# Optimization experiments

Measured on AMD Instinct MI355X. Metric: run time of the kernel, lower is better.

Reference implementation:

```python
import jax, jax.numpy as jnp
import numpy as np

B, S, D_IN, HID, H, OUT = 4, 2048, 1024, 1024, 16, 128
DH = HID // H
SCALE = float(np.sqrt(DH))
ELEV, FLOOR2 = 4, 32


def setup_inputs() -> dict:
    key = jax.random.key(0)
    ks = jax.random.split(key, 12)
    w = lambda k, o, i: jax.random.normal(k, (o, i), dtype=jnp.float32) * 0.02
    b = lambda k, o: jax.random.normal(k, (o,), dtype=jnp.float32) * 0.02
    return {
        "query": jax.random.normal(ks[0], (B, S, D_IN), dtype=jnp.float32),
        "key": jax.random.normal(ks[1], (B, S, D_IN), dtype=jnp.float32),
        "value": jax.random.normal(ks[2], (B, S, D_IN), dtype=jnp.float32),
        "mask": jax.random.randint(ks[3], (B, 1, 1, S), 0, 2, dtype=jnp.int32),
        "wq_w": w(ks[4], HID, D_IN), "wq_b": b(ks[5], HID),
        "wk_w": w(ks[6], HID, D_IN), "wk_b": b(ks[7], HID),
        "wv_w": w(ks[8], HID, D_IN), "wv_b": b(ks[9], HID),
        "fc_w": w(ks[10], OUT, HID), "fc_b": b(ks[11], OUT),
    }


def reference(query, key, value, mask, wq_w, wq_b, wk_w, wk_b, wv_w, wv_b, fc_w, fc_b):
    bsz, seq = query.shape[0], query.shape[1]
    # torch Linear: x @ W.T + b
    split = lambda x: x.reshape(bsz, seq, H, DH).transpose(0, 2, 1, 3)  # (b,h,s,dh)
    Q = split(query @ wq_w.T + wq_b)
    K = split(key @ wk_w.T + wk_b)
    V = split(value @ wv_w.T + wv_b)
    energy = jnp.einsum('bhqd,bhkd->bhqk', Q, K) / SCALE
    energy = jnp.where(mask == 0, jnp.float32(-1e10), energy)
    attn = jax.nn.softmax(energy, axis=-1)  # dropout is identity in eval mode
    x = jnp.einsum('bhqk,bhkd->bhqd', attn, V)
    x = x.transpose(0, 2, 1, 3).reshape(bsz, seq, HID)
    x = x @ fc_w.T + fc_b
    x = x.reshape(-1, ELEV, FLOOR2)  # (b*s, elevator_num, floor_num*2)
    return jax.nn.softmax(x, axis=1)  # nn.Softmax(dim=1)
```

## Files before the change

kernel.cpp:

```cpp
#include <hip/hip_runtime.h>
#include <stdint.h>

#define S_LEN 2048
#define DK 1024
#define NH 16
#define DH 64
#define LOG2E 1.4426950408889634f
#define M_FIX 10.0f

typedef __attribute__((ext_vector_type(8))) short bf16x8;
typedef __attribute__((ext_vector_type(4))) float f32x4;

__device__ __forceinline__ unsigned short f2bf(float f) {
    union { float f; uint32_t u; } v; v.f = f;
    return (unsigned short)((v.u + 0x7fffu + ((v.u >> 16) & 1u)) >> 16);
}

__device__ __forceinline__ float fast_exp2(float x) {
#if __has_builtin(__builtin_amdgcn_exp2f)
    return __builtin_amdgcn_exp2f(x);
#else
    return exp2f(x);
#endif
}

__device__ __forceinline__ uint32_t cvt_pk_bf16(float a, float b) {
    uint32_t r;
    asm("v_cvt_pk_bf16_f32 %0, %1, %2" : "=v"(r) : "v"(a), "v"(b));
    return r;
}

__device__ __forceinline__ void gload_lds16(const void* g, void* l) {
    __builtin_amdgcn_global_load_lds((const __attribute__((address_space(1))) void*)g,
                                     (__attribute__((address_space(3))) void*)l, 16, 0, 0);
}

__global__ __launch_bounds__(256) void cvt7_kernel(
    const float* __restrict__ a0, const float* __restrict__ a1, const float* __restrict__ a2,
    const float* __restrict__ a3, const float* __restrict__ a4, const float* __restrict__ a5,
    const float* __restrict__ a6,
    unsigned short* __restrict__ o0, unsigned short* __restrict__ o1, unsigned short* __restrict__ o2,
    unsigned short* __restrict__ o3, unsigned short* __restrict__ o4, unsigned short* __restrict__ o5,
    unsigned short* __restrict__ o6,
    int n4_big, int n4_w, int n4_f)
{
    const int y = blockIdx.y;
    const float* in = (y == 0) ? a0 : (y == 1) ? a1 : (y == 2) ? a2 :
                      (y == 3) ? a3 : (y == 4) ? a4 : (y == 5) ? a5 : a6;
    unsigned short* out = (y == 0) ? o0 : (y == 1) ? o1 : (y == 2) ? o2 :
                          (y == 3) ? o3 : (y == 4) ? o4 : (y == 5) ? o5 : o6;
    const int n4 = (y < 3) ? n4_big : ((y < 6) ? n4_w : n4_f);
    const float4* pin = (const float4*)in;
    ushort4* pout = (ushort4*)out;
    int i = blockIdx.x * blockDim.x + threadIdx.x;
    int stride = gridDim.x * blockDim.x;
    for (; i < n4; i += stride) {
        float4 v = pin[i];
        ushort4 o;
        o.x = f2bf(v.x); o.y = f2bf(v.y); o.z = f2bf(v.z); o.w = f2bf(v.w);
        pout[i] = o;
    }
}

__global__ __launch_bounds__(512) void proj_gemm(
    const unsigned short* __restrict__ Xq, const unsigned short* __restrict__ Xk, const unsigned short* __restrict__ Xv,
    const unsigned short* __restrict__ Wq, const unsigned short* __restrict__ Wk, const unsigned short* __restrict__ Wv,
    const float* __restrict__ bq, const float* __restrict__ bk, const float* __restrict__ bv,
    unsigned short* __restrict__ Qh, unsigned short* __restrict__ Kh, unsigned short* __restrict__ Vt)
{
    const int d = blockIdx.x + (blockIdx.y << 3) + (blockIdx.z << 9);
    const int k = d & 7, s = d >> 3;
    const int nn = s & 7;
    const int mz = ((s >> 3) << 3) + k;
    const int m0 = (mz & 63) * 128;
    const int z = mz >> 6;

    const unsigned short* X = (z == 0) ? Xq : ((z == 1) ? Xk : Xv);
    const unsigned short* W = (z == 0) ? Wq : ((z == 1) ? Wk : Wv);
    const float* bias = (z == 0) ? bq : ((z == 1) ? bk : bv);

    const int n0 = nn * 128;
    const int tid = threadIdx.x;
    const int w = tid >> 6;
    const int l = tid & 63;
    const int wm = w >> 2, wn = w & 3;
    const int g = l >> 4, c = l & 15;

    __shared__ __align__(16) unsigned short As[2][2 * 128 * 32];
    __shared__ __align__(16) unsigned short Bs[2][2 * 128 * 32];

    f32x4 acc[4][2] = {};

    const int srow = l >> 2;
    const int schunk = (((l & 3) - (l >> 3)) & 3) * 8;

    const int sub = w >> 2;
    const int rb = 32 * (w & 3);

    auto stage = [&](int kk, int buf) {
#pragma unroll
        for (int i = 0; i < 2; ++i) {
            int r0 = rb + 16 * i;
            gload_lds16(X + (size_t)(m0 + r0 + srow) * DK + kk + 32 * sub + schunk,
                        &As[buf][sub * 4096 + r0 * 32]);
            gload_lds16(W + (size_t)(n0 + r0 + srow) * DK + kk + 32 * sub + schunk,
                        &Bs[buf][sub * 4096 + r0 * 32]);
        }
    };

    stage(0, 0);

    for (int t = 0; t < 16; ++t) {
        const int buf = t & 1;
        __syncthreads();

        if (t < 15) stage((t + 1) << 6, buf ^ 1);

        const int rchunk = 8 * ((g + (c >> 1)) & 3);
        __builtin_amdgcn_s_setprio(1);
#pragma unroll
        for (int k32 = 0; k32 < 2; ++k32) {
            bf16x8 a[4], bb[2];
#pragma unroll
            for (int mi = 0; mi < 4; ++mi)
                a[mi] = *(const bf16x8*)&As[buf][k32 * 4096 + (64 * wm + 16 * mi + c) * 32 + rchunk];
#pragma unroll
            for (int nj = 0; nj < 2; ++nj)
                bb[nj] = *(const bf16x8*)&Bs[buf][k32 * 4096 + (32 * wn + 16 * nj + c) * 32 + rchunk];
#pragma unroll
            for (int mi = 0; mi < 4; ++mi)
#pragma unroll
                for (int nj = 0; nj < 2; ++nj)
                    acc[mi][nj] = __builtin_amdgcn_mfma_f32_16x16x32_bf16(a[mi], bb[nj], acc[mi][nj], 0, 0, 0);
        }
        __builtin_amdgcn_s_setprio(0);
    }

    const float scale = (z == 0) ? (0.125f * LOG2E) : 1.0f;
#pragma unroll
    for (int mi = 0; mi < 4; ++mi) {
#pragma unroll
        for (int nj = 0; nj < 2; ++nj) {
            int col = n0 + 32 * wn + 16 * nj + c;
            float bval = bias[col];
            int h = col >> 6, dh = col & 63;
            int row0 = m0 + 64 * wm + 16 * mi + 4 * g;
            int b = row0 >> 11, ss = row0 & 2047;
            if (z != 2) {
                unsigned short* Out = (z == 0) ? Qh : Kh;
#pragma unroll
                for (int r = 0; r < 4; ++r) {
                    float v = (acc[mi][nj][r] + bval) * scale;
                    Out[((size_t)(b * NH + h) * S_LEN + (ss + r)) * DH + dh] = f2bf(v);
                }
            } else {
                ushort4 o;
                o.x = f2bf(acc[mi][nj][0] + bval);
                o.y = f2bf(acc[mi][nj][1] + bval);
                o.z = f2bf(acc[mi][nj][2] + bval);
                o.w = f2bf(acc[mi][nj][3] + bval);
                int q = (ss >> 2) & 7;
                int newpos = (ss & ~31) + 8 * (q & 3) + 4 * (q >> 2);
                *(ushort4*)&Vt[((size_t)(b * NH + h) * DH + dh) * S_LEN + newpos] = o;
            }
        }
    }
}

__global__ __launch_bounds__(256, 4) void attn_kernel(
    const unsigned short* __restrict__ Qh, const unsigned short* __restrict__ Kh,
    const unsigned short* __restrict__ Vt, const int* __restrict__ maskI,
    unsigned short* __restrict__ O)
{
    const int id = blockIdx.x + (blockIdx.y << 4);
    const int swzid = (id & 7) * 128 + (id >> 3);
    const int q0 = (swzid & 15) * 128;
    const int bh = swzid >> 4;
    const int b = bh >> 4, h = bh & 15;
    const int tid = threadIdx.x, w = tid >> 6, l = tid & 63;
    const int g = l >> 4, c = l & 15;

    __shared__ __align__(16) unsigned short Ks[2][4096];
    __shared__ __align__(16) unsigned short Vs[2][4096];
    __shared__ __align__(16) float mskA[S_LEN];

    bf16x8 qf[2][2];
    const size_t qbase = (size_t)bh * S_LEN + q0 + 32 * w;
#pragma unroll
    for (int mi = 0; mi < 2; ++mi)
#pragma unroll
        for (int k32 = 0; k32 < 2; ++k32)
            qf[mi][k32] = *(const bf16x8*)&Qh[(qbase + 16 * mi + c) * DH + k32 * 32 + 8 * g];

    f32x4 ao[2][4] = {};
    f32x4 ls[2] = {};
    bf16x8 ones;
#pragma unroll
    for (int j = 0; j < 8; ++j) ones[j] = (short)0x3F80;

    const int kswz = ((l & 7) ^ (l >> 3)) * 8;
    const int vrow = l >> 2;
    const int vsrc = (((l & 3) - (l >> 3)) & 3) * 8;

    auto stageKV = [&](int kv, int buf) {
#pragma unroll
        for (int u = 0; u < 2; ++u) {
            int kvs = kv + 32 * u;
            gload_lds16(Kh + ((size_t)bh * S_LEN + kvs + 8 * w + (l >> 3)) * DH + kswz,
                        &Ks[buf][u * 2048 + w * 512]);
            gload_lds16(Vt + ((size_t)bh * DH + 16 * w + vrow) * S_LEN + kvs + vsrc,
                        &Vs[buf][u * 2048 + w * 512]);
        }
    };

    stageKV(0, 0);
    {
        const int4* mp = (const int4*)(maskI + b * S_LEN);
#pragma unroll
        for (int i = 0; i < 2; ++i) {
            int idx = tid + 256 * i;
            int4 m = mp[idx];
            float4 f;
            f.x = m.x ? (-M_FIX * LOG2E) : -3e38f;
            f.y = m.y ? (-M_FIX * LOG2E) : -3e38f;
            f.z = m.z ? (-M_FIX * LOG2E) : -3e38f;
            f.w = m.w ? (-M_FIX * LOG2E) : -3e38f;
            *(float4*)&mskA[idx * 4] = f;
        }
    }

    for (int t = 0; t < 32; ++t) {
        const int cur = t & 1;
        const int kv0 = t << 6;
        __syncthreads();

        if (t < 31) stageKV(kv0 + 64, cur ^ 1);

#pragma unroll
        for (int u = 0; u < 2; ++u) {
            const int base = u * 2048;
            const int kv0s = kv0 + 32 * u;

            float4 mk0 = *(const float4*)&mskA[kv0s + 4 * g];
            float4 mk1 = *(const float4*)&mskA[kv0s + 16 + 4 * g];
            f32x4 sf[2][2];
            sf[0][0] = f32x4{mk0.x, mk0.y, mk0.z, mk0.w};
            sf[1][0] = sf[0][0];
            sf[0][1] = f32x4{mk1.x, mk1.y, mk1.z, mk1.w};
            sf[1][1] = sf[0][1];

            __builtin_amdgcn_s_setprio(1);
#pragma unroll
            for (int nj = 0; nj < 2; ++nj) {
                int krow = 16 * nj + c;
#pragma unroll
                for (int k32 = 0; k32 < 2; ++k32) {
                    int chunk = (k32 * 4 + g) ^ (krow & 7);
                    bf16x8 kf = *(const bf16x8*)&Ks[cur][base + krow * 64 + chunk * 8];
#pragma unroll
                    for (int mi = 0; mi < 2; ++mi)
                        sf[mi][nj] = __builtin_amdgcn_mfma_f32_16x16x32_bf16(kf, qf[mi][k32], sf[mi][nj], 0, 0, 0);
                }
            }
            __builtin_amdgcn_s_setprio(0);

            bf16x8 pf[2];
#pragma unroll
            for (int mi = 0; mi < 2; ++mi) {
                float e00 = fast_exp2(sf[mi][0][0]);
                float e01 = fast_exp2(sf[mi][0][1]);
                float e02 = fast_exp2(sf[mi][0][2]);
                float e03 = fast_exp2(sf[mi][0][3]);
                float e10 = fast_exp2(sf[mi][1][0]);
                float e11 = fast_exp2(sf[mi][1][1]);
                float e12 = fast_exp2(sf[mi][1][2]);
                float e13 = fast_exp2(sf[mi][1][3]);
                union { uint32_t u2[4]; bf16x8 v; } pu;
                pu.u2[0] = cvt_pk_bf16(e00, e01);
                pu.u2[1] = cvt_pk_bf16(e02, e03);
                pu.u2[2] = cvt_pk_bf16(e10, e11);
                pu.u2[3] = cvt_pk_bf16(e12, e13);
                pf[mi] = pu.v;
            }

            __builtin_amdgcn_s_setprio(1);
#pragma unroll
            for (int nc = 0; nc < 4; ++nc) {
                int row = 16 * nc + c;
                int s16 = (g + (c >> 1)) & 3;
                bf16x8 vf = *(const bf16x8*)&Vs[cur][base + row * 32 + 8 * s16];
#pragma unroll
                for (int mi = 0; mi < 2; ++mi)
                    ao[mi][nc] = __builtin_amdgcn_mfma_f32_16x16x32_bf16(pf[mi], vf, ao[mi][nc], 0, 0, 0);
            }
#pragma unroll
            for (int mi = 0; mi < 2; ++mi)
                ls[mi] = __builtin_amdgcn_mfma_f32_16x16x32_bf16(pf[mi], ones, ls[mi], 0, 0, 0);
            __builtin_amdgcn_s_setprio(0);
        }
    }

#pragma unroll
    for (int mi = 0; mi < 2; ++mi)
#pragma unroll
        for (int r = 0; r < 4; ++r) {
            int s = q0 + 32 * w + 16 * mi + 4 * g + r;
            float inv = 1.0f / ls[mi][r];
#pragma unroll
            for (int nc = 0; nc < 4; ++nc) {
                int dh = 16 * nc + c;
                O[(size_t)(b * S_LEN + s) * 1024 + h * DH + dh] = f2bf(ao[mi][nc][r] * inv);
            }
        }
}

__global__ __launch_bounds__(256) void fc_kernel(
    const unsigned short* __restrict__ O, const unsigned short* __restrict__ Wf,
    const float* __restrict__ bfc, float* __restrict__ out)
{
    const int m0 = blockIdx.x * 64;
    const int tid = threadIdx.x, w = tid >> 6, l = tid & 63;
    const int g = l >> 4, c = l & 15;

    __shared__ __align__(16) unsigned short As[3][64 * 32];
    __shared__ __align__(16) unsigned short Bs[3][128 * 32];

    f32x4 acc[8] = {};

    const int srow = l >> 2;
    const int schunk = (((l & 3) - (l >> 3)) & 3) * 8;

    auto stage = [&](int kk, int buf) {
        gload_lds16(O + (size_t)(m0 + 16 * w + srow) * DK + kk + schunk, &As[buf][16 * w * 32]);
#pragma unroll
        for (int j = 0; j < 2; ++j) {
            int r0 = 32 * w + 16 * j;
            gload_lds16(Wf + (size_t)(r0 + srow) * DK + kk + schunk, &Bs[buf][r0 * 32]);
        }
    };

    stage(0, 0);
    stage(32, 1);

    int cur = 0;
    for (int step = 0; step < 32; ++step) {
        if (step < 31) asm volatile("s_waitcnt vmcnt(3)" ::: "memory");
        else           asm volatile("s_waitcnt vmcnt(0)" ::: "memory");
        __builtin_amdgcn_s_barrier();
        __builtin_amdgcn_sched_barrier(0);

        if (step < 30) {
            int nb = cur + 2; if (nb >= 3) nb -= 3;
            stage((step + 2) << 5, nb);
        }

        const int rchunk = 8 * ((g + (c >> 1)) & 3);
        bf16x8 a = *(const bf16x8*)&As[cur][(16 * w + c) * 32 + rchunk];
        bf16x8 bb[8];
#pragma unroll
        for (int nj = 0; nj < 8; ++nj)
            bb[nj] = *(const bf16x8*)&Bs[cur][(16 * nj + c) * 32 + rchunk];
        __builtin_amdgcn_s_setprio(1);
#pragma unroll
        for (int nj = 0; nj < 8; ++nj)
            acc[nj] = __builtin_amdgcn_mfma_f32_16x16x32_bf16(a, bb[nj], acc[nj], 0, 0, 0);
        __builtin_amdgcn_s_setprio(0);

        ++cur; if (cur == 3) cur = 0;
    }

#pragma unroll
    for (int r = 0; r < 4; ++r) {
        int row = m0 + 16 * w + (l >> 4) * 4 + r;
#pragma unroll
        for (int par = 0; par < 2; ++par) {
            float v[4];
#pragma unroll
            for (int e = 0; e < 4; ++e) {
                int col = 16 * (2 * e + par) + (l & 15);
                v[e] = acc[2 * e + par][r] + bfc[col];
            }
            float mx = fmaxf(fmaxf(v[0], v[1]), fmaxf(v[2], v[3]));
            float ex[4], ssum = 0.f;
#pragma unroll
            for (int e = 0; e < 4; ++e) { ex[e] = fast_exp2((v[e] - mx) * LOG2E); ssum += ex[e]; }
            float inv = 1.0f / ssum;
#pragma unroll
            for (int e = 0; e < 4; ++e) {
                int col = 16 * (2 * e + par) + (l & 15);
                out[(size_t)row * 128 + col] = ex[e] * inv;
            }
        }
    }
}

extern "C" void kernel_launch(void* const* d_in, const int* in_sizes, int n_in,
                              void* d_out, int out_size, void* d_ws, size_t ws_size,
                              hipStream_t stream) {
    (void)in_sizes; (void)n_in; (void)out_size; (void)ws_size;
    const float* q    = (const float*)d_in[0];
    const float* k    = (const float*)d_in[1];
    const float* v    = (const float*)d_in[2];
    const int*   mask = (const int*)d_in[3];
    const float* wq_w = (const float*)d_in[4];
    const float* wq_b = (const float*)d_in[5];
    const float* wk_w = (const float*)d_in[6];
    const float* wk_b = (const float*)d_in[7];
    const float* wv_w = (const float*)d_in[8];
    const float* wv_b = (const float*)d_in[9];
    const float* fc_w = (const float*)d_in[10];
    const float* fc_b = (const float*)d_in[11];

    const size_t NX = (size_t)8192 * 1024;
    const size_t NW = (size_t)1024 * 1024;
    const size_t NF = (size_t)128 * 1024;

    unsigned short* Xq = (unsigned short*)d_ws;
    unsigned short* Xk = Xq + NX;
    unsigned short* Xv = Xk + NX;
    unsigned short* Wq = Xv + NX;
    unsigned short* Wk = Wq + NW;
    unsigned short* Wv = Wk + NW;
    unsigned short* Wf = Wv + NW;
    unsigned short* Qh = Wf + NF;
    unsigned short* Kh = Qh + NX;
    unsigned short* Vt = Kh + NX;
    unsigned short* O  = Xq;

    cvt7_kernel<<<dim3(2048, 7), 256, 0, stream>>>(q, k, v, wq_w, wk_w, wv_w, fc_w,
                                                   Xq, Xk, Xv, Wq, Wk, Wv, Wf,
                                                   (int)(NX / 4), (int)(NW / 4), (int)(NF / 4));

    proj_gemm<<<dim3(8, 64, 3), 512, 0, stream>>>(Xq, Xk, Xv, Wq, Wk, Wv,
                                                  wq_b, wk_b, wv_b, Qh, Kh, Vt);
    attn_kernel<<<dim3(16, 64), 256, 0, stream>>>(Qh, Kh, Vt, mask, O);
    fc_kernel<<<128, 256, 0, stream>>>(O, Wf, fc_b, (float*)d_out);
}
```

Before: 178.6 us.

## Triple-buffer A tiles in QKV projection GEMM with explicit vmcnt waits

In the QKV projection GEMM, the A (activation) tile goes from double to triple buffering and is prefetched two k-steps ahead, while the B (weight) tile stays double-buffered. The full __syncthreads is replaced by an explicit s_waitcnt vmcnt(2) plus s_barrier, so the newest A prefetch can still be in flight while the current step computes. The aim is to hide more global-load latency behind the MFMA work. In exchange, LDS per block grows from 64 KB to 80 KB, and correctness now depends on the hand-counted outstanding-load ordering.

```diff
diff --git a/kernel.cpp b/kernel.cpp
--- a/kernel.cpp
+++ b/kernel.cpp
@@ -86,7 +86,7 @@
     const int wm = w >> 2, wn = w & 3;
     const int g = l >> 4, c = l & 15;
 
-    __shared__ __align__(16) unsigned short As[2][2 * 128 * 32];
+    __shared__ __align__(16) unsigned short As[3][2 * 128 * 32];
     __shared__ __align__(16) unsigned short Bs[2][2 * 128 * 32];
 
     f32x4 acc[4][2] = {};
@@ -97,25 +97,41 @@
     const int sub = w >> 2;
     const int rb = 32 * (w & 3);
 
-    auto stage = [&](int kk, int buf) {
+    auto stageA = [&](int kk, int buf) {
 #pragma unroll
         for (int i = 0; i < 2; ++i) {
             int r0 = rb + 16 * i;
             gload_lds16(X + (size_t)(m0 + r0 + srow) * DK + kk + 32 * sub + schunk,
                         &As[buf][sub * 4096 + r0 * 32]);
+        }
+    };
+    auto stageB = [&](int kk, int buf) {
+#pragma unroll
+        for (int i = 0; i < 2; ++i) {
+            int r0 = rb + 16 * i;
             gload_lds16(W + (size_t)(n0 + r0 + srow) * DK + kk + 32 * sub + schunk,
                         &Bs[buf][sub * 4096 + r0 * 32]);
         }
     };
 
-    stage(0, 0);
-
+    stageA(0, 0);
+    stageB(0, 0);
+    stageA(64, 1);
+
+    int aCur = 0;
     for (int t = 0; t < 16; ++t) {
-        const int buf = t & 1;
-        __syncthreads();
-
-        if (t < 15) stage((t + 1) << 6, buf ^ 1);
-
+        if (t < 15) asm volatile("s_waitcnt vmcnt(2)" ::: "memory");
+        else        asm volatile("s_waitcnt vmcnt(0)" ::: "memory");
+        __builtin_amdgcn_s_barrier();
+        __builtin_amdgcn_sched_barrier(0);
+
+        if (t < 15) stageB((t + 1) << 6, (t + 1) & 1);
+        if (t < 14) {
+            int nb = aCur + 2; if (nb >= 3) nb -= 3;
+            stageA((t + 2) << 6, nb);
+        }
+
+        const int bbuf = t & 1;
         const int rchunk = 8 * ((g + (c >> 1)) & 3);
         __builtin_amdgcn_s_setprio(1);
 #pragma unroll
@@ -123,10 +139,10 @@
             bf16x8 a[4], bb[2];
 #pragma unroll
             for (int mi = 0; mi < 4; ++mi)
-                a[mi] = *(const bf16x8*)&As[buf][k32 * 4096 + (64 * wm + 16 * mi + c) * 32 + rchunk];
+                a[mi] = *(const bf16x8*)&As[aCur][k32 * 4096 + (64 * wm + 16 * mi + c) * 32 + rchunk];
 #pragma unroll
             for (int nj = 0; nj < 2; ++nj)
-                bb[nj] = *(const bf16x8*)&Bs[buf][k32 * 4096 + (32 * wn + 16 * nj + c) * 32 + rchunk];
+                bb[nj] = *(const bf16x8*)&Bs[bbuf][k32 * 4096 + (32 * wn + 16 * nj + c) * 32 + rchunk];
 #pragma unroll
             for (int mi = 0; mi < 4; ++mi)
 #pragma unroll
@@ -134,6 +150,8 @@
                     acc[mi][nj] = __builtin_amdgcn_mfma_f32_16x16x32_bf16(a[mi], bb[nj], acc[mi][nj], 0, 0, 0);
         }
         __builtin_amdgcn_s_setprio(0);
+
+        ++aCur; if (aCur == 3) aCur = 0;
     }
 
     const float scale = (z == 0) ? (0.125f * LOG2E) : 1.0f;
```

After: 178.9 us. About the same (+0.2%).
